# Performance work log

Measured on AMD Instinct MI355X. Metric: run time of the kernel, lower is better.

The kernel has to match this reference:

```python
import jax, jax.numpy as jnp
from jax import lax
import numpy as np

B, S, D = 32, 2048, 512

def setup_inputs() -> dict:
    key = jax.random.key(0)
    ks = jax.random.split(key, 9)
    inv = 1.0 / np.sqrt(D).astype(np.float32)
    return {
        "query": jax.random.normal(ks[0], (B, 1, D), jnp.float32),
        "value": jax.random.normal(ks[1], (B, S, D), jnp.float32),
        "last_alignment_energy": jax.random.uniform(ks[2], (B, S), jnp.float32),
        "conv_w": jax.random.normal(ks[3], (D, 1, 3), jnp.float32) * 0.1,  # Conv1d(1->D,k=3)
        "conv_b": jax.random.normal(ks[4], (D,), jnp.float32) * 0.01,
        "w_q": jax.random.normal(ks[5], (D, D), jnp.float32) * inv,  # applied as x @ w_q
        "w_v": jax.random.normal(ks[6], (D, D), jnp.float32) * inv,
        "bias": jax.random.uniform(ks[7], (D,), jnp.float32, minval=-0.1, maxval=0.1),
        "score_w": jax.random.normal(ks[8], (D,), jnp.float32) * inv,  # score_proj weight (out=1)
        "score_b": jnp.zeros((), jnp.float32),
    }


def reference(query, value, last_alignment_energy, conv_w, conv_b, w_q, w_v, bias, score_w, score_b):
    # location features: Conv1d(1->D, k=3, pad=1) over the previous alignment
    loc = lax.conv_general_dilated(
        last_alignment_energy[:, None, :], conv_w,
        window_strides=(1,), padding=[(1, 1)],
        dimension_numbers=("NCH", "OIH", "NCH"))  # [B, D, S]
    loc = jnp.transpose(loc, (0, 2, 1)) + conv_b  # [B, S, D]

    # additive attention energy: tanh(Wq q + Wv v + loc + b) @ score_w
    hidden = jnp.tanh(query @ w_q + value @ w_v + loc + bias)  # [B, S, D] (query broadcasts over S)
    scores = hidden @ score_w + score_b                          # [B, S]
    align = jax.nn.softmax(scores, axis=-1)                      # [B, S]

    # context = align^T V
    context = jnp.einsum("bs,bsd->bd", align, value)             # [B, D]
    return context, align
```

## Files before the change

### kernel.cpp

```cpp
#include <hip/hip_runtime.h>
#include <hip/hip_bf16.h>

#define B_ 32
#define S_ 2048
#define D_ 512
#define M_ (B_*S_)
#define KS_ 16

typedef __bf16 bf16x8 __attribute__((ext_vector_type(8)));
typedef float  f32x4  __attribute__((ext_vector_type(4)));

__device__ __forceinline__ float tanh_fast(float x){
  float e2 = __expf(2.f * x);
  return 1.f - 2.f * __builtin_amdgcn_rcpf(e2 + 1.f);
}
__device__ __forceinline__ float b2f(unsigned short u){
  unsigned int x = ((unsigned int)u) << 16;
  return __builtin_bit_cast(float, x);
}
__device__ __forceinline__ bf16x8 cvt8(f32x4 a, f32x4 b){
  bf16x8 t;
  t[0]=(__bf16)a[0]; t[1]=(__bf16)a[1]; t[2]=(__bf16)a[2]; t[3]=(__bf16)a[3];
  t[4]=(__bf16)b[0]; t[5]=(__bf16)b[1]; t[6]=(__bf16)b[2]; t[7]=(__bf16)b[3];
  return t;
}
__device__ __forceinline__ void gl_lds16(const void* g, void* l){
  __builtin_amdgcn_global_load_lds(
      (const __attribute__((address_space(1))) unsigned int*)g,
      (__attribute__((address_space(3))) unsigned int*)l, 16, 0, 0);
}

__global__ void k_prep(const float* __restrict__ value, unsigned short* __restrict__ valueb,
                       const float* __restrict__ wv, unsigned short* __restrict__ wvr2,
                       const float* __restrict__ q, const float* __restrict__ wq,
                       const float* __restrict__ bias, float* __restrict__ qp){
  __shared__ float qs[D_];
  __shared__ float red[2][128];
  const int bi = blockIdx.x, t = threadIdx.x;
  if (bi < 4096){
    size_t base = (size_t)bi * 8192;
    #pragma unroll
    for (int i=0;i<4;++i){
      size_t idx = base + (size_t)(i*256 + t)*8;
      f32x4 a = *reinterpret_cast<const f32x4*>(value + idx);
      f32x4 b = *reinterpret_cast<const f32x4*>(value + idx + 4);
      *reinterpret_cast<uint4*>(valueb + idx) = __builtin_bit_cast(uint4, cvt8(a,b));
    }
  } else if (bi < 4224){
    int g = (bi-4096)*256 + t;
    int lane = g & 63, frag = g >> 6;
    int ntl = frag & 7, nh = (frag>>3)&3, ks = frag>>5;
    int nt = nh*8 + ntl;
    int k0 = ks*32 + (lane>>4)*8;
    int d  = nt*16 + (lane&15);
    bf16x8 v;
    #pragma unroll
    for (int j=0;j<8;++j) v[j] = (__bf16)wv[(size_t)(k0+j)*D_ + d];
    *reinterpret_cast<uint4*>(wvr2 + ((size_t)frag*64 + lane)*8) =
        __builtin_bit_cast(uint4, v);
  } else {
    int j  = bi - 4224;
    int b  = j >> 2, dg = j & 3;
    int dl = t & 127, eg = t >> 7;
    int d  = dg*128 + dl;
    for (int e=t; e<D_; e+=256) qs[e] = q[b*D_+e];
    __syncthreads();
    float acc = 0.f;
    #pragma unroll 8
    for (int i=0;i<256;++i){
      int e = eg*256 + i;
      acc = fmaf(qs[e], wq[(size_t)e*D_+d], acc);
    }
    red[eg][dl] = acc;
    __syncthreads();
    if (eg == 0)
      qp[b*D_+d] = red[0][dl] + red[1][dl] + bias[d];
  }
}

__launch_bounds__(256)
__global__ void k_energy(const unsigned short* __restrict__ valueb,
                         const unsigned short* __restrict__ wvr2,
                         const float* __restrict__ qp,
                         const float* __restrict__ energy,
                         const float* __restrict__ conv_w,
                         const float* __restrict__ conv_b,
                         const float* __restrict__ score_w,
                         float* __restrict__ sp){
  __shared__ __align__(16) unsigned short As[2][4096];
  __shared__ __align__(16) unsigned short Bs[2][4096];
  __shared__ float red[2][128];

  const int t    = threadIdx.x;
  const int wave = t >> 6;
  const int lane = t & 63;
  const int quad = lane >> 4;
  const int lm   = lane & 15;
  const int wh   = wave & 1;
  const int wc   = wave >> 1;
  const int rt   = blockIdx.x >> 2;
  const int nh   = blockIdx.x & 3;
  const int row0 = rt * 128;
  const int b    = row0 >> 11;
  const int s0   = row0 & (S_-1);

  const unsigned short* gA0 = valueb + (size_t)(row0 + (t>>2))*D_
                                     + ((t&3) ^ ((t>>2)&3))*8;
  const unsigned short* gA1 = gA0 + (size_t)64*D_;
  const unsigned short* gB  = wvr2 + (size_t)nh*4096 + t*8;

  f32x4 acc[4][4];
  #pragma unroll
  for (int mt=0;mt<4;++mt)
    #pragma unroll
    for (int nt=0;nt<4;++nt)
      acc[mt][nt] = (f32x4){0.f,0.f,0.f,0.f};

  gl_lds16(gA0, &As[0][t*8]);
  gl_lds16(gA1, &As[0][2048 + t*8]);
  gl_lds16(gB,        &Bs[0][t*8]);
  gl_lds16(gB + 2048, &Bs[0][2048 + t*8]);
  __syncthreads();

  for (int ks=0; ks<KS_; ++ks){
    const int buf = ks & 1;
    if (ks < KS_-1){
      gl_lds16(gA0 + (ks+1)*32, &As[buf^1][t*8]);
      gl_lds16(gA1 + (ks+1)*32, &As[buf^1][2048 + t*8]);
      gl_lds16(gB + (ks+1)*16384,        &Bs[buf^1][t*8]);
      gl_lds16(gB + (ks+1)*16384 + 2048, &Bs[buf^1][2048 + t*8]);
    }
    const unsigned short* Ab = &As[buf][0];
    const unsigned short* Bb = &Bs[buf][0];
    bf16x8 a[4], bf[4];
    #pragma unroll
    for (int mt=0;mt<4;++mt){
      int arow = wh*64 + mt*16 + lm;
      a[mt] = *reinterpret_cast<const bf16x8*>(
                &Ab[arow*32 + ((quad ^ (lm&3)))*8]);
    }
    #pragma unroll
    for (int nt=0;nt<4;++nt)
      bf[nt] = *reinterpret_cast<const bf16x8*>(
                &Bb[((wc*4+nt)*64 + lane)*8]);
    #pragma unroll
    for (int mt=0;mt<4;++mt)
      #pragma unroll
      for (int nt=0;nt<4;++nt)
        acc[mt][nt] = __builtin_amdgcn_mfma_f32_16x16x32_bf16(a[mt], bf[nt], acc[mt][nt], 0,0,0);
    __syncthreads();
  }

  float sw[4], c0[4], c1[4], c2[4], cb[4], qv[4];
  #pragma unroll
  for (int nt=0; nt<4; ++nt){
    int d = nh*128 + wc*64 + nt*16 + lm;
    sw[nt] = score_w[d];
    c0[nt] = conv_w[d*3+0];
    c1[nt] = conv_w[d*3+1];
    c2[nt] = conv_w[d*3+2];
    cb[nt] = conv_b[d];
    qv[nt] = qp[b*D_+d];
  }
  const float* eB = energy + b*S_;
  #pragma unroll
  for (int mt=0; mt<4; ++mt){
    #pragma unroll
    for (int r=0;r<4;++r){
      int sl = wh*64 + mt*16 + quad*4 + r;
      int s  = s0 + sl;
      float em1 = (s > 0)    ? eB[s-1] : 0.f;
      float e0  =              eB[s];
      float ep1 = (s < S_-1) ? eB[s+1] : 0.f;
      float p = 0.f;
      #pragma unroll
      for (int nt=0; nt<4; ++nt){
        float h = acc[mt][nt][r] + qv[nt]
                + fmaf(c0[nt],em1, fmaf(c1[nt],e0, fmaf(c2[nt],ep1, cb[nt])));
        p = fmaf(sw[nt], tanh_fast(h), p);
      }
      #pragma unroll
      for (int m=1; m<16; m<<=1) p += __shfl_xor(p, m, 64);
      if (lm == 0) red[wc][sl] = p;
    }
  }
  __syncthreads();
  if (t < 128)
    sp[(size_t)nh*M_ + row0 + t] = red[0][t] + red[1][t];
}

__global__ void k_softmax(const float* __restrict__ sp,
                          float* __restrict__ out_align){
  int b = blockIdx.x, t = threadIdx.x;
  int lane = t & 63, wid = t >> 6;
  float v[8], mx = -3.4e38f;
  #pragma unroll
  for (int i=0;i<8;++i){
    int s = t + i*256;
    float sc = sp[0*M_+b*S_+s] + sp[1*M_+b*S_+s] + sp[2*M_+b*S_+s] + sp[3*M_+b*S_+s];
    v[i] = sc;
    mx = fmaxf(mx, sc);
  }
  __shared__ float red[4], red2[4];
  #pragma unroll
  for (int m=1;m<64;m<<=1) mx = fmaxf(mx, __shfl_xor(mx, m, 64));
  if (lane==0) red[wid] = mx;
  __syncthreads();
  mx = fmaxf(fmaxf(red[0],red[1]), fmaxf(red[2],red[3]));
  float sum = 0.f;
  #pragma unroll
  for (int i=0;i<8;++i){ v[i] = __expf(v[i]-mx); sum += v[i]; }
  #pragma unroll
  for (int m=1;m<64;m<<=1) sum += __shfl_xor(sum, m, 64);
  if (lane==0) red2[wid] = sum;
  __syncthreads();
  sum = red2[0]+red2[1]+red2[2]+red2[3];
  float inv = 1.f/sum;
  #pragma unroll
  for (int i=0;i<8;++i) out_align[b*S_ + t + i*256] = v[i]*inv;
}

__launch_bounds__(512)
__global__ void k_ctx(const unsigned short* __restrict__ valueb,
                      const float* __restrict__ align,
                      float* __restrict__ cpart){
  int b = blockIdx.y, sc = blockIdx.x;
  int t = threadIdx.x;
  int r = t >> 6;
  int c = (t & 63) * 8;
  __shared__ float als[128];
  __shared__ float lred[8][D_];
  if (t < 128) als[t] = align[b*S_ + sc*128 + t];
  __syncthreads();
  float acc[8] = {0,0,0,0,0,0,0,0};
  #pragma unroll 4
  for (int i=0;i<16;++i){
    int sl = i*8 + r;
    float al = als[sl];
    uint4 u = *reinterpret_cast<const uint4*>(
                valueb + ((size_t)(b*S_ + sc*128 + sl))*D_ + c);
    unsigned short tt[8]; __builtin_memcpy(tt, &u, 16);
    #pragma unroll
    for (int j=0;j<8;++j) acc[j] = fmaf(al, b2f(tt[j]), acc[j]);
  }
  #pragma unroll
  for (int j=0;j<8;++j) lred[r][c+j] = acc[j];
  __syncthreads();
  if (r == 0){
    #pragma unroll
    for (int j=0;j<8;++j){
      float s = 0.f;
      #pragma unroll
      for (int k=0;k<8;++k) s += lred[k][c+j];
      cpart[((size_t)(b*16+sc))*D_ + c + j] = s;
    }
  }
}

__global__ void k_ctx_reduce(const float* __restrict__ cpart,
                             float* __restrict__ out_ctx){
  int idx = blockIdx.x*256 + threadIdx.x;
  int b = idx >> 9, d = idx & 511;
  float s = 0.f;
  #pragma unroll
  for (int j=0;j<16;++j) s += cpart[((size_t)(b*16+j))*D_ + d];
  out_ctx[idx] = s;
}

extern "C" void kernel_launch(void* const* d_in, const int* in_sizes, int n_in,
                              void* d_out, int out_size, void* d_ws, size_t ws_size,
                              hipStream_t stream){
  const float* query   = (const float*)d_in[0];
  const float* value   = (const float*)d_in[1];
  const float* energy  = (const float*)d_in[2];
  const float* conv_w  = (const float*)d_in[3];
  const float* conv_b  = (const float*)d_in[4];
  const float* w_q     = (const float*)d_in[5];
  const float* w_v     = (const float*)d_in[6];
  const float* bias    = (const float*)d_in[7];
  const float* score_w = (const float*)d_in[8];

  char* ws = (char*)d_ws;
  unsigned short* valueb = (unsigned short*)(ws);
  unsigned short* wvr2   = (unsigned short*)(ws + ((size_t)65536<<10));
  float* qp     = (float*)(ws + ((size_t)66048<<10));
  float* sp     = (float*)(ws + ((size_t)66112<<10));
  float* cpart  = (float*)(ws + ((size_t)67136<<10));

  float* out_ctx   = (float*)d_out;
  float* out_align = out_ctx + B_*D_;

  k_prep      <<<dim3(4352),      dim3(256), 0, stream>>>(value, valueb, w_v, wvr2,
                                                          query, w_q, bias, qp);
  k_energy    <<<dim3(2048),      dim3(256), 0, stream>>>(valueb, wvr2, qp, energy,
                                                          conv_w, conv_b, score_w, sp);
  k_softmax   <<<dim3(B_),        dim3(256), 0, stream>>>(sp, out_align);
  k_ctx       <<<dim3(16,B_),     dim3(512), 0, stream>>>(valueb, out_align, cpart);
  k_ctx_reduce<<<dim3(B_*D_/256), dim3(256), 0, stream>>>(cpart, out_ctx);
}
```

Measured before the change: 304.7 us.

## Drop bf16 value prepass; convert fp32 value on the fly in GEMM and context

Removes the full-tensor fp32-to-bf16 conversion of value from the prep kernel. The energy GEMM now loads fp32 value tiles into LDS with a new swizzle and converts them to bf16 when building MFMA fragments, and the context kernel reads fp32 value directly. This eliminates a large read-plus-write pass over value. In exchange, the GEMM and context kernels read twice as many bytes for A and the A LDS footprint doubles, which may reduce occupancy.

```diff
diff --git a/kernel.cpp b/kernel.cpp
--- a/kernel.cpp
+++ b/kernel.cpp
@@ -14,10 +14,6 @@
   float e2 = __expf(2.f * x);
   return 1.f - 2.f * __builtin_amdgcn_rcpf(e2 + 1.f);
 }
-__device__ __forceinline__ float b2f(unsigned short u){
-  unsigned int x = ((unsigned int)u) << 16;
-  return __builtin_bit_cast(float, x);
-}
 __device__ __forceinline__ bf16x8 cvt8(f32x4 a, f32x4 b){
   bf16x8 t;
   t[0]=(__bf16)a[0]; t[1]=(__bf16)a[1]; t[2]=(__bf16)a[2]; t[3]=(__bf16)a[3];
@@ -30,24 +26,14 @@
       (__attribute__((address_space(3))) unsigned int*)l, 16, 0, 0);
 }
 
-__global__ void k_prep(const float* __restrict__ value, unsigned short* __restrict__ valueb,
-                       const float* __restrict__ wv, unsigned short* __restrict__ wvr2,
+__global__ void k_prep(const float* __restrict__ wv, unsigned short* __restrict__ wvr2,
                        const float* __restrict__ q, const float* __restrict__ wq,
                        const float* __restrict__ bias, float* __restrict__ qp){
   __shared__ float qs[D_];
   __shared__ float red[2][128];
   const int bi = blockIdx.x, t = threadIdx.x;
-  if (bi < 4096){
-    size_t base = (size_t)bi * 8192;
-    #pragma unroll
-    for (int i=0;i<4;++i){
-      size_t idx = base + (size_t)(i*256 + t)*8;
-      f32x4 a = *reinterpret_cast<const f32x4*>(value + idx);
-      f32x4 b = *reinterpret_cast<const f32x4*>(value + idx + 4);
-      *reinterpret_cast<uint4*>(valueb + idx) = __builtin_bit_cast(uint4, cvt8(a,b));
-    }
-  } else if (bi < 4224){
-    int g = (bi-4096)*256 + t;
+  if (bi < 128){
+    int g = bi*256 + t;
     int lane = g & 63, frag = g >> 6;
     int ntl = frag & 7, nh = (frag>>3)&3, ks = frag>>5;
     int nt = nh*8 + ntl;
@@ -59,7 +45,7 @@
     *reinterpret_cast<uint4*>(wvr2 + ((size_t)frag*64 + lane)*8) =
         __builtin_bit_cast(uint4, v);
   } else {
-    int j  = bi - 4224;
+    int j  = bi - 128;
     int b  = j >> 2, dg = j & 3;
     int dl = t & 127, eg = t >> 7;
     int d  = dg*128 + dl;
@@ -79,7 +65,7 @@
 }
 
 __launch_bounds__(256)
-__global__ void k_energy(const unsigned short* __restrict__ valueb,
+__global__ void k_energy(const float* __restrict__ value,
                          const unsigned short* __restrict__ wvr2,
                          const float* __restrict__ qp,
                          const float* __restrict__ energy,
@@ -87,7 +73,7 @@
                          const float* __restrict__ conv_b,
                          const float* __restrict__ score_w,
                          float* __restrict__ sp){
-  __shared__ __align__(16) unsigned short As[2][4096];
+  __shared__ __align__(16) float          As[2][4096];
   __shared__ __align__(16) unsigned short Bs[2][4096];
   __shared__ float red[2][128];
 
@@ -104,10 +90,15 @@
   const int b    = row0 >> 11;
   const int s0   = row0 & (S_-1);
 
-  const unsigned short* gA0 = valueb + (size_t)(row0 + (t>>2))*D_
-                                     + ((t&3) ^ ((t>>2)&3))*8;
-  const unsigned short* gA1 = gA0 + (size_t)64*D_;
-  const unsigned short* gB  = wvr2 + (size_t)nh*4096 + t*8;
+  const float* gA[4];
+  #pragma unroll
+  for (int i=0;i<4;++i){
+    int u   = i*256 + t;
+    int row = u >> 3;
+    int dc  = (u & 7) ^ (row & 7);
+    gA[i] = value + (size_t)(row0 + row)*D_ + dc*4;
+  }
+  const unsigned short* gB = wvr2 + (size_t)nh*4096 + t*8;
 
   f32x4 acc[4][4];
   #pragma unroll
@@ -116,8 +107,8 @@
     for (int nt=0;nt<4;++nt)
       acc[mt][nt] = (f32x4){0.f,0.f,0.f,0.f};
 
-  gl_lds16(gA0, &As[0][t*8]);
-  gl_lds16(gA1, &As[0][2048 + t*8]);
+  #pragma unroll
+  for (int i=0;i<4;++i) gl_lds16(gA[i], &As[0][(i*256 + t)*4]);
   gl_lds16(gB,        &Bs[0][t*8]);
   gl_lds16(gB + 2048, &Bs[0][2048 + t*8]);
   __syncthreads();
@@ -125,24 +116,26 @@
   for (int ks=0; ks<KS_; ++ks){
     const int buf = ks & 1;
     if (ks < KS_-1){
-      gl_lds16(gA0 + (ks+1)*32, &As[buf^1][t*8]);
-      gl_lds16(gA1 + (ks+1)*32, &As[buf^1][2048 + t*8]);
+      #pragma unroll
+      for (int i=0;i<4;++i) gl_lds16(gA[i] + (ks+1)*32, &As[buf^1][(i*256 + t)*4]);
       gl_lds16(gB + (ks+1)*16384,        &Bs[buf^1][t*8]);
       gl_lds16(gB + (ks+1)*16384 + 2048, &Bs[buf^1][2048 + t*8]);
     }
-    const unsigned short* Ab = &As[buf][0];
+    const float* Ab = &As[buf][0];
     const unsigned short* Bb = &Bs[buf][0];
     bf16x8 a[4], bf[4];
     #pragma unroll
     for (int mt=0;mt<4;++mt){
-      int arow = wh*64 + mt*16 + lm;
-      a[mt] = *reinterpret_cast<const bf16x8*>(
-                &Ab[arow*32 + ((quad ^ (lm&3)))*8]);
+      int arow  = wh*64 + mt*16 + lm;
+      int slot0 = (quad*2)     ^ (lm & 7);
+      int slot1 = (quad*2 + 1) ^ (lm & 7);
+      f32x4 p0 = *reinterpret_cast<const f32x4*>(&Ab[arow*32 + slot0*4]);
+      f32x4 p1 = *reinterpret_cast<const f32x4*>(&Ab[arow*32 + slot1*4]);
+      a[mt] = cvt8(p0, p1);
     }
     #pragma unroll
     for (int nt=0;nt<4;++nt)
-      bf[nt] = *reinterpret_cast<const bf16x8*>(
-                &Bb[((wc*4+nt)*64 + lane)*8]);
+      bf[nt] = *reinterpret_cast<const bf16x8*>(&Bb[((wc*4+nt)*64 + lane)*8]);
     #pragma unroll
     for (int mt=0;mt<4;++mt)
       #pragma unroll
@@ -221,39 +214,34 @@
 }
 
 __launch_bounds__(512)
-__global__ void k_ctx(const unsigned short* __restrict__ valueb,
+__global__ void k_ctx(const float* __restrict__ value,
                       const float* __restrict__ align,
                       float* __restrict__ cpart){
   int b = blockIdx.y, sc = blockIdx.x;
   int t = threadIdx.x;
-  int r = t >> 6;
-  int c = (t & 63) * 8;
+  int r = t >> 7;
+  int c = (t & 127) * 4;
   __shared__ float als[128];
-  __shared__ float lred[8][D_];
+  __shared__ float lred[4][D_];
   if (t < 128) als[t] = align[b*S_ + sc*128 + t];
   __syncthreads();
-  float acc[8] = {0,0,0,0,0,0,0,0};
-  #pragma unroll 4
-  for (int i=0;i<16;++i){
-    int sl = i*8 + r;
+  f32x4 acc = (f32x4){0.f,0.f,0.f,0.f};
+  #pragma unroll 8
+  for (int i=0;i<32;++i){
+    int sl = i*4 + r;
     float al = als[sl];
-    uint4 u = *reinterpret_cast<const uint4*>(
-                valueb + ((size_t)(b*S_ + sc*128 + sl))*D_ + c);
-    unsigned short tt[8]; __builtin_memcpy(tt, &u, 16);
-    #pragma unroll
-    for (int j=0;j<8;++j) acc[j] = fmaf(al, b2f(tt[j]), acc[j]);
-  }
-  #pragma unroll
-  for (int j=0;j<8;++j) lred[r][c+j] = acc[j];
+    f32x4 vv = *reinterpret_cast<const f32x4*>(
+                 value + ((size_t)(b*S_ + sc*128 + sl))*D_ + c);
+    acc += al * vv;
+  }
+  #pragma unroll
+  for (int j=0;j<4;++j) lred[r][c+j] = acc[j];
   __syncthreads();
   if (r == 0){
     #pragma unroll
-    for (int j=0;j<8;++j){
-      float s = 0.f;
-      #pragma unroll
-      for (int k=0;k<8;++k) s += lred[k][c+j];
-      cpart[((size_t)(b*16+sc))*D_ + c + j] = s;
-    }
+    for (int j=0;j<4;++j)
+      cpart[((size_t)(b*16+sc))*D_ + c + j] =
+          lred[0][c+j] + lred[1][c+j] + lred[2][c+j] + lred[3][c+j];
   }
 }
 
@@ -281,20 +269,18 @@
   const float* score_w = (const float*)d_in[8];
 
   char* ws = (char*)d_ws;
-  unsigned short* valueb = (unsigned short*)(ws);
-  unsigned short* wvr2   = (unsigned short*)(ws + ((size_t)65536<<10));
-  float* qp     = (float*)(ws + ((size_t)66048<<10));
-  float* sp     = (float*)(ws + ((size_t)66112<<10));
-  float* cpart  = (float*)(ws + ((size_t)67136<<10));
+  unsigned short* wvr2 = (unsigned short*)(ws);
+  float* qp    = (float*)(ws + (512<<10));
+  float* sp    = (float*)(ws + (576<<10));
+  float* cpart = (float*)(ws + (1600<<10));
 
   float* out_ctx   = (float*)d_out;
   float* out_align = out_ctx + B_*D_;
 
-  k_prep      <<<dim3(4352),      dim3(256), 0, stream>>>(value, valueb, w_v, wvr2,
-                                                          query, w_q, bias, qp);
-  k_energy    <<<dim3(2048),      dim3(256), 0, stream>>>(valueb, wvr2, qp, energy,
+  k_prep      <<<dim3(256),       dim3(256), 0, stream>>>(w_v, wvr2, query, w_q, bias, qp);
+  k_energy    <<<dim3(2048),      dim3(256), 0, stream>>>(value, wvr2, qp, energy,
                                                           conv_w, conv_b, score_w, sp);
   k_softmax   <<<dim3(B_),        dim3(256), 0, stream>>>(sp, out_align);
-  k_ctx       <<<dim3(16,B_),     dim3(512), 0, stream>>>(valueb, out_align, cpart);
+  k_ctx       <<<dim3(16,B_),     dim3(512), 0, stream>>>(value, out_align, cpart);
   k_ctx_reduce<<<dim3(B_*D_/256), dim3(256), 0, stream>>>(cpart, out_ctx);
 }
```

Measured after the change: 325.7 us. +6.9%, slower.
